# Performance work log

Hardware: AMD Instinct MI355X
Metric: run time of the kernel (lower is better)

## Reference

```python
import jax, jax.numpy as jnp
import numpy as np

MARGIN = 1.0
EPS = 1e-6


def _cos(a, b):
    # Row-wise cosine similarity, matching torch.nn.CosineSimilarity semantics:
    # dot / max(||a|| * ||b||, eps)
    num = jnp.sum(a * b, axis=-1)
    den = jnp.maximum(jnp.linalg.norm(a, axis=-1) * jnp.linalg.norm(b, axis=-1), EPS)
    return num / den


def setup_inputs() -> dict:
    key = jax.random.key(0)
    k1, k2, k3 = jax.random.split(key, 3)
    B, D = 16384, 1024
    output = jax.random.normal(k1, (B, D), dtype=jnp.float32)
    target = jax.random.normal(k2, (B, D), dtype=jnp.float32)
    # offset in [0, B-1); j = (i + 1 + neg_idx) % B guarantees j != i, uniform over the rest
    neg_idx = jax.random.randint(k3, (B,), 0, B - 1, dtype=jnp.int64)
    return {"output": output, "target": target, "neg_idx": neg_idx}


def reference(output, target, neg_idx):
    B = output.shape[0]
    j = (jnp.arange(B) + 1 + neg_idx) % B  # random negative index, j != i
    t_neg = target[j]                       # gather negative label embeddings [B, D]
    hinge = jax.nn.relu(MARGIN - _cos(target, output) + _cos(t_neg, output))
    return jnp.sum(hinge) / B
```

## Files before the change

kernel.cpp:

```cpp
#include <hip/hip_runtime.h>
#include <hip/hip_bf16.h>


#define EPS 1e-6f

typedef float f4 __attribute__((ext_vector_type(4)));

#define WAIT_VM0   0x0f70
#define WAIT_LGKM0 0xc07f

#define DPP_STEP(x, ctrl, rm, bm)                                             \
    x += __int_as_float(__builtin_amdgcn_update_dpp(                          \
        0, __float_as_int(x), (ctrl), (rm), (bm), true))

__device__ __forceinline__ float dpp_wave_sum(float x) {
    DPP_STEP(x, 0x111, 0xf, 0xf);
    DPP_STEP(x, 0x112, 0xf, 0xf);
    DPP_STEP(x, 0x114, 0xf, 0xe);
    DPP_STEP(x, 0x118, 0xf, 0xc);
    DPP_STEP(x, 0x142, 0xa, 0xf);
    DPP_STEP(x, 0x143, 0xc, 0xf);
    return x;
}

__device__ __forceinline__ void dma16(const float* g, float* l) {
    __builtin_amdgcn_global_load_lds(
        (const __attribute__((address_space(1))) float*)g,
        (__attribute__((address_space(3))) float*)l,
        16, 0, 0);
}

__global__ __launch_bounds__(256, 3) void hinge_cos_kernel(
    const float* __restrict__ outm,
    const float* __restrict__ tgt,
    const int*   __restrict__ negidx,
    float* __restrict__ res,
    int B, int D, float invB) {

    __shared__ float stage[4][3072];
    __shared__ float red[4];

    const int lane  = threadIdx.x & 63;
    const int wave  = threadIdx.x >> 6;
    const int gwave = blockIdx.x * 4 + wave;
    const int nwav  = gridDim.x * 4;

    float* sw = &stage[wave][0];
    const f4* sv = (const f4*)sw;

    float acc = 0.f;

    for (int i = gwave; i < B; i += nwav) {
        int j = i + 1 + negidx[i];
        if (j >= B) j -= B;

        const float* ob = outm + (size_t)i * D;
        const float* tb = tgt  + (size_t)i * D;
        const float* nb = tgt  + (size_t)j * D;

        __builtin_amdgcn_s_waitcnt(WAIT_LGKM0);

#pragma unroll
        for (int k = 0; k < 4; ++k) dma16(ob + k * 256 + lane * 4, sw + k * 256);
#pragma unroll
        for (int k = 0; k < 4; ++k) dma16(tb + k * 256 + lane * 4, sw + 1024 + k * 256);
#pragma unroll
        for (int k = 0; k < 4; ++k) dma16(nb + k * 256 + lane * 4, sw + 2048 + k * 256);

        __builtin_amdgcn_s_waitcnt(WAIT_VM0);
        __builtin_amdgcn_sched_barrier(0);

        float dto = 0.f, dno = 0.f, oo = 0.f, tt = 0.f, nn = 0.f;
#pragma unroll
        for (int k = 0; k < 4; ++k) {
            f4 o = sv[      k * 64 + lane];
            f4 t = sv[256 + k * 64 + lane];
            f4 n = sv[512 + k * 64 + lane];
            dto += o.x * t.x + o.y * t.y + o.z * t.z + o.w * t.w;
            dno += o.x * n.x + o.y * n.y + o.z * n.z + o.w * n.w;
            oo  += o.x * o.x + o.y * o.y + o.z * o.z + o.w * o.w;
            tt  += t.x * t.x + t.y * t.y + t.z * t.z + t.w * t.w;
            nn  += n.x * n.x + n.y * n.y + n.z * n.z + n.w * n.w;
        }

        dto = dpp_wave_sum(dto);
        dno = dpp_wave_sum(dno);
        oo  = dpp_wave_sum(oo);
        tt  = dpp_wave_sum(tt);
        nn  = dpp_wave_sum(nn);

        if (lane == 63) {
            float no = sqrtf(oo);
            float h  = 1.f - dto / fmaxf(sqrtf(tt) * no, EPS)
                           + dno / fmaxf(sqrtf(nn) * no, EPS);
            acc += fmaxf(h, 0.f);
        }
    }

    if (lane == 63) red[wave] = acc;
    __syncthreads();
    if (threadIdx.x == 0) {
        float s = 0.f;
#pragma unroll
        for (int w = 0; w < 4; ++w) s += red[w];
        atomicAdd(res, s * invB);
    }
}

extern "C" void kernel_launch(void* const* d_in, const int* in_sizes, int n_in,
                              void* d_out, int out_size, void* d_ws, size_t ws_size,
                              hipStream_t stream) {
    const float* outm   = (const float*)d_in[0];
    const float* tgt    = (const float*)d_in[1];
    const int*   negidx = (const int*)d_in[2];
    float* res = (float*)d_out;

    const int B = in_sizes[2];
    const int D = in_sizes[0] / B;

    (void)hipMemsetAsync(res, 0, sizeof(float), stream);

    hinge_cos_kernel<<<768, 256, 0, stream>>>(outm, tgt, negidx, res, B, D,
                                              1.0f / (float)B);
}
```

Baseline: 151.3 us.

## Replace LDS DMA staging with register double-buffered loads, four rows per wave

Drops the global_load_lds staging and its blocking waitcnt in favor of direct vector loads into registers, double-buffered so a wave keeps two rows in flight and overlaps the next row's loads with the current row's reductions. For D=1024 and B divisible by 16, a specialized kernel launches B/16 blocks, each wave handling exactly four rows with no loop, and the output rows use nontemporal loads. Frees LDS, which allows higher occupancy, but uses more registers per wave; a generic loop kernel is kept as a fallback.

```diff
diff --git a/kernel.cpp b/kernel.cpp
--- a/kernel.cpp
+++ b/kernel.cpp
@@ -5,9 +5,6 @@
 #define EPS 1e-6f
 
 typedef float f4 __attribute__((ext_vector_type(4)));
-
-#define WAIT_VM0   0x0f70
-#define WAIT_LGKM0 0xc07f
 
 #define DPP_STEP(x, ctrl, rm, bm)                                             \
     x += __int_as_float(__builtin_amdgcn_update_dpp(                          \
@@ -23,86 +20,104 @@
     return x;
 }
 
-__device__ __forceinline__ void dma16(const float* g, float* l) {
-    __builtin_amdgcn_global_load_lds(
-        (const __attribute__((address_space(1))) float*)g,
-        (__attribute__((address_space(3))) float*)l,
-        16, 0, 0);
+struct Buf { f4 o[4], t[4], n[4]; };
+
+__device__ __forceinline__ void issue(Buf& b,
+                                      const float* __restrict__ ob,
+                                      const float* __restrict__ tb,
+                                      const float* __restrict__ nb,
+                                      int lane) {
+#pragma unroll
+    for (int k = 0; k < 4; ++k)
+        b.o[k] = __builtin_nontemporal_load((const f4*)ob + lane + 64 * k);
+#pragma unroll
+    for (int k = 0; k < 4; ++k) b.t[k] = *((const f4*)tb + lane + 64 * k);
+#pragma unroll
+    for (int k = 0; k < 4; ++k) b.n[k] = *((const f4*)nb + lane + 64 * k);
 }
 
-__global__ __launch_bounds__(256, 3) void hinge_cos_kernel(
-    const float* __restrict__ outm,
-    const float* __restrict__ tgt,
-    const int*   __restrict__ negidx,
-    float* __restrict__ res,
+__device__ __forceinline__ float consume(const Buf& b) {
+    float dto = 0.f, dno = 0.f, oo = 0.f, tt = 0.f, nn = 0.f;
+#pragma unroll
+    for (int k = 0; k < 4; ++k) {
+        dto += b.o[k].x*b.t[k].x + b.o[k].y*b.t[k].y + b.o[k].z*b.t[k].z + b.o[k].w*b.t[k].w;
+        dno += b.o[k].x*b.n[k].x + b.o[k].y*b.n[k].y + b.o[k].z*b.n[k].z + b.o[k].w*b.n[k].w;
+        oo  += b.o[k].x*b.o[k].x + b.o[k].y*b.o[k].y + b.o[k].z*b.o[k].z + b.o[k].w*b.o[k].w;
+        tt  += b.t[k].x*b.t[k].x + b.t[k].y*b.t[k].y + b.t[k].z*b.t[k].z + b.t[k].w*b.t[k].w;
+        nn  += b.n[k].x*b.n[k].x + b.n[k].y*b.n[k].y + b.n[k].z*b.n[k].z + b.n[k].w*b.n[k].w;
+    }
+    dto = dpp_wave_sum(dto);
+    dno = dpp_wave_sum(dno);
+    oo  = dpp_wave_sum(oo);
+    tt  = dpp_wave_sum(tt);
+    nn  = dpp_wave_sum(nn);
+    float no = sqrtf(oo);
+    float h  = 1.f - dto / fmaxf(sqrtf(tt) * no, EPS)
+                   + dno / fmaxf(sqrtf(nn) * no, EPS);
+    return fmaxf(h, 0.f);
+}
+
+__global__ __launch_bounds__(256, 4) void hinge_cos_pipe4(
+    const float* __restrict__ outm, const float* __restrict__ tgt,
+    const int* __restrict__ negidx, float* __restrict__ res,
     int B, int D, float invB) {
 
-    __shared__ float stage[4][3072];
+    const int lane  = threadIdx.x & 63;
+    const int wave  = threadIdx.x >> 6;
+    const int gwave = blockIdx.x * 4 + wave;
+    const int nw    = gridDim.x * 4;
+
+    const int r0 = gwave, r1 = gwave + nw, r2 = gwave + 2 * nw, r3 = gwave + 3 * nw;
+    int j0 = r0 + 1 + negidx[r0]; if (j0 >= B) j0 -= B;
+    int j1 = r1 + 1 + negidx[r1]; if (j1 >= B) j1 -= B;
+    int j2 = r2 + 1 + negidx[r2]; if (j2 >= B) j2 -= B;
+    int j3 = r3 + 1 + negidx[r3]; if (j3 >= B) j3 -= B;
+
+    Buf A, Bb;
+    issue(A,  outm + (size_t)r0 * D, tgt + (size_t)r0 * D, tgt + (size_t)j0 * D, lane);
+    issue(Bb, outm + (size_t)r1 * D, tgt + (size_t)r1 * D, tgt + (size_t)j1 * D, lane);
+    __builtin_amdgcn_sched_barrier(0);
+    float acc = consume(A);
+    issue(A,  outm + (size_t)r2 * D, tgt + (size_t)r2 * D, tgt + (size_t)j2 * D, lane);
+    __builtin_amdgcn_sched_barrier(0);
+    acc += consume(Bb);
+    issue(Bb, outm + (size_t)r3 * D, tgt + (size_t)r3 * D, tgt + (size_t)j3 * D, lane);
+    __builtin_amdgcn_sched_barrier(0);
+    acc += consume(A);
+    acc += consume(Bb);
+
     __shared__ float red[4];
+    if (lane == 63) red[wave] = acc;
+    __syncthreads();
+    if (threadIdx.x == 0) {
+        float s = red[0] + red[1] + red[2] + red[3];
+        atomicAdd(res, s * invB);
+    }
+}
+
+__global__ __launch_bounds__(256, 8) void hinge_cos_generic(
+    const float* __restrict__ outm, const float* __restrict__ tgt,
+    const int* __restrict__ negidx, float* __restrict__ res,
+    int B, int D, float invB) {
 
     const int lane  = threadIdx.x & 63;
     const int wave  = threadIdx.x >> 6;
     const int gwave = blockIdx.x * 4 + wave;
     const int nwav  = gridDim.x * 4;
 
-    float* sw = &stage[wave][0];
-    const f4* sv = (const f4*)sw;
-
     float acc = 0.f;
-
     for (int i = gwave; i < B; i += nwav) {
         int j = i + 1 + negidx[i];
         if (j >= B) j -= B;
-
-        const float* ob = outm + (size_t)i * D;
-        const float* tb = tgt  + (size_t)i * D;
-        const float* nb = tgt  + (size_t)j * D;
-
-        __builtin_amdgcn_s_waitcnt(WAIT_LGKM0);
-
-#pragma unroll
-        for (int k = 0; k < 4; ++k) dma16(ob + k * 256 + lane * 4, sw + k * 256);
-#pragma unroll
-        for (int k = 0; k < 4; ++k) dma16(tb + k * 256 + lane * 4, sw + 1024 + k * 256);
-#pragma unroll
-        for (int k = 0; k < 4; ++k) dma16(nb + k * 256 + lane * 4, sw + 2048 + k * 256);
-
-        __builtin_amdgcn_s_waitcnt(WAIT_VM0);
-        __builtin_amdgcn_sched_barrier(0);
-
-        float dto = 0.f, dno = 0.f, oo = 0.f, tt = 0.f, nn = 0.f;
-#pragma unroll
-        for (int k = 0; k < 4; ++k) {
-            f4 o = sv[      k * 64 + lane];
-            f4 t = sv[256 + k * 64 + lane];
-            f4 n = sv[512 + k * 64 + lane];
-            dto += o.x * t.x + o.y * t.y + o.z * t.z + o.w * t.w;
-            dno += o.x * n.x + o.y * n.y + o.z * n.z + o.w * n.w;
-            oo  += o.x * o.x + o.y * o.y + o.z * o.z + o.w * o.w;
-            tt  += t.x * t.x + t.y * t.y + t.z * t.z + t.w * t.w;
-            nn  += n.x * n.x + n.y * n.y + n.z * n.z + n.w * n.w;
-        }
-
-        dto = dpp_wave_sum(dto);
-        dno = dpp_wave_sum(dno);
-        oo  = dpp_wave_sum(oo);
-        tt  = dpp_wave_sum(tt);
-        nn  = dpp_wave_sum(nn);
-
-        if (lane == 63) {
-            float no = sqrtf(oo);
-            float h  = 1.f - dto / fmaxf(sqrtf(tt) * no, EPS)
-                           + dno / fmaxf(sqrtf(nn) * no, EPS);
-            acc += fmaxf(h, 0.f);
-        }
+        Buf b;
+        issue(b, outm + (size_t)i * D, tgt + (size_t)i * D, tgt + (size_t)j * D, lane);
+        acc += consume(b);
     }
-
+    __shared__ float red[4];
     if (lane == 63) red[wave] = acc;
     __syncthreads();
     if (threadIdx.x == 0) {
-        float s = 0.f;
-#pragma unroll
-        for (int w = 0; w < 4; ++w) s += red[w];
+        float s = red[0] + red[1] + red[2] + red[3];
         atomicAdd(res, s * invB);
     }
 }
@@ -120,6 +135,11 @@
 
     (void)hipMemsetAsync(res, 0, sizeof(float), stream);
 
-    hinge_cos_kernel<<<768, 256, 0, stream>>>(outm, tgt, negidx, res, B, D,
-                                              1.0f / (float)B);
+    if (D == 1024 && (B % 16) == 0) {
+        hinge_cos_pipe4<<<B / 16, 256, 0, stream>>>(outm, tgt, negidx, res,
+                                                    B, D, 1.0f / (float)B);
+    } else {
+        hinge_cos_generic<<<2048, 256, 0, stream>>>(outm, tgt, negidx, res,
+                                                    B, D, 1.0f / (float)B);
+    }
 }
```

Measured after the change: 146.5 us. 3.1% less time.
